# Kernel tuning notes

Hardware: AMD Instinct MI355X
Metric: run time of the kernel (lower is better)

## Reference

```python
import jax, jax.numpy as jnp
import numpy as np

N_NODES = 50000
N_EDGES = 800000
EMB = 100
LAYERS = 3
EPS = 1e-12  # torch F.normalize default eps


def setup_inputs() -> dict:
    key = jax.random.key(0)
    k1, k2, k3, k4 = jax.random.split(key, 4)
    adj_row = jax.random.randint(k1, (N_EDGES,), 0, N_NODES, dtype=jnp.int32)
    adj_col = jax.random.randint(k2, (N_EDGES,), 0, N_NODES, dtype=jnp.int32)
    adj_val = jax.random.uniform(k3, (N_EDGES,), dtype=jnp.float32)
    embedding = jax.random.normal(k4, (N_NODES, EMB), dtype=jnp.float32)
    a = jnp.ones((LAYERS + 1, 1, 1), dtype=jnp.float32)  # init.ones_
    return {"adj_row": adj_row, "adj_col": adj_col, "adj_val": adj_val,
            "embedding": embedding, "a": a}


def reference(adj_row, adj_col, adj_val, embedding, a):
    def spmm(x):
        # sparse.mm(A, x): gather source rows, scale by edge value, scatter-add to dest rows
        return jax.ops.segment_sum(adj_val[:, None] * x[adj_col], adj_row,
                                   num_segments=N_NODES)

    outs = [embedding]
    x = embedding
    for _ in range(LAYERS):
        x = spmm(x)
        outs.append(x)
    final = jnp.stack(outs, axis=0)  # [L+1, N, d]
    # F.normalize(..., dim=-1, p=2): x / max(||x||_2, eps)
    norm = jnp.sqrt(jnp.sum(final * final, axis=-1, keepdims=True))
    final = final / jnp.maximum(norm, EPS)
    return jnp.sum(a * final, axis=0)  # [N, d]
```

## Files before the change

kernel.cpp:

```cpp
#include <hip/hip_runtime.h>
#include <hip/hip_bf16.h>

#define N_NODES 50000
#define N_EDGES 800000
#define EMB 100
#define HALF_EMB 50
#define QEMB 25
#define NORM_EPS 1e-12f
#define BROWS 128
#define NB ((N_NODES + BROWS - 1) / BROWS)
#define CAP 4096
#define EPB 4096
#define SCAT_BLOCKS ((N_EDGES + EPB - 1) / EPB)
#define CONV_BLOCKS 3125

__global__ __launch_bounds__(1024) void scatter_conv(
        const int* __restrict__ adj_row, const int* __restrict__ adj_col,
        const float* __restrict__ adj_val, int* __restrict__ bucket_cnt,
        int2* __restrict__ slab,
        const float* __restrict__ emb, float* __restrict__ norm0,
        __hip_bfloat162* __restrict__ xb) {
    const int t = threadIdx.x;
    if (blockIdx.x >= SCAT_BLOCKS) {
        int wave = (blockIdx.x - SCAT_BLOCKS) * 16 + (t >> 6);
        int lane = t & 63;
        if (wave >= N_NODES) return;
        float2 v = make_float2(0.0f, 0.0f);
        size_t idx = (size_t)wave * HALF_EMB + lane;
        if (lane < HALF_EMB) v = ((const float2*)emb)[idx];
        float s = v.x * v.x + v.y * v.y;
        #pragma unroll
        for (int off = 32; off > 0; off >>= 1) s += __shfl_xor(s, off);
        if (lane == 0) norm0[wave] = sqrtf(s);
        if (lane < HALF_EMB) {
            __hip_bfloat162 b;
            b.x = __float2bfloat16(v.x);
            b.y = __float2bfloat16(v.y);
            xb[idx] = b;
        }
        return;
    }
    __shared__ int hist[NB];
    __shared__ int cur[NB];
    const int base_e = blockIdx.x * EPB;
    for (int i = t; i < NB; i += 1024) hist[i] = 0;
    __syncthreads();
    int rows[EPB / 1024];
    #pragma unroll
    for (int j = 0; j < EPB / 1024; ++j) {
        int e = base_e + j * 1024 + t;
        int r = (e < N_EDGES) ? adj_row[e] : -1;
        rows[j] = r;
        if (r >= 0) atomicAdd(&hist[r >> 7], 1);
    }
    __syncthreads();
    for (int i = t; i < NB; i += 1024) {
        int c = hist[i];
        cur[i] = (c > 0) ? atomicAdd(&bucket_cnt[i], c) : 0;
    }
    __syncthreads();
    #pragma unroll
    for (int j = 0; j < EPB / 1024; ++j) {
        int e = base_e + j * 1024 + t;
        int r = rows[j];
        if (r >= 0) {
            int b = r >> 7;
            int p = atomicAdd(&cur[b], 1);
            unsigned rc = ((unsigned)r << 16) | (unsigned)adj_col[e];
            slab[(size_t)b * CAP + p] = make_int2((int)rc, __float_as_int(adj_val[e]));
        }
    }
}

__global__ __launch_bounds__(1024) void csr_build(
        const int* __restrict__ bucket_cnt, const int2* __restrict__ slab,
        unsigned* __restrict__ csr4, int* __restrict__ row_ptr) {
    __shared__ int2 eds[CAP];
    __shared__ int hist[BROWS];
    __shared__ int incl[BROWS];
    __shared__ int red[1024];
    const int b = blockIdx.x, t = threadIdx.x;
    red[t] = (t < b) ? bucket_cnt[t] : 0;
    __syncthreads();
    #pragma unroll
    for (int off = 512; off > 0; off >>= 1) {
        if (t < off) red[t] += red[t + off];
        __syncthreads();
    }
    const int base = red[0];
    const int cnt = bucket_cnt[b];
    for (int i = t; i < cnt; i += 1024) eds[i] = slab[(size_t)b * CAP + i];
    if (t < BROWS) hist[t] = 0;
    __syncthreads();
    for (int i = t; i < cnt; i += 1024)
        atomicAdd(&hist[(int)(((unsigned)eds[i].x) >> 16) & (BROWS - 1)], 1);
    __syncthreads();
    int v = (t < BROWS) ? hist[t] : 0;
    if (t < BROWS) incl[t] = v;
    __syncthreads();
    #pragma unroll
    for (int off = 1; off < BROWS; off <<= 1) {
        int n = (t >= off && t < BROWS) ? incl[t - off] : 0;
        __syncthreads();
        if (t < BROWS) incl[t] += n;
        __syncthreads();
    }
    int ex = (t < BROWS) ? (incl[t] - v) : 0;
    __syncthreads();
    if (t < BROWS) hist[t] = ex;
    int gr = b * BROWS + t;
    if (t < BROWS && gr < N_NODES) row_ptr[gr] = base + ex;
    if (b == 0 && t == 0) row_ptr[N_NODES] = N_EDGES;
    __syncthreads();
    for (int i = t; i < cnt; i += 1024) {
        int2 e = eds[i];
        int l = (int)(((unsigned)e.x) >> 16) & (BROWS - 1);
        int p = atomicAdd(&hist[l], 1);
        unsigned col = (unsigned)e.x & 0xFFFFu;
        __hip_bfloat16 hv = __float2bfloat16(__int_as_float(e.y));
        unsigned vb = (unsigned)*reinterpret_cast<unsigned short*>(&hv);
        csr4[base + p] = (col << 16) | vb;
    }
}

__device__ inline float4 up4(uint2 u) {
    float4 f;
    f.x = __uint_as_float(u.x << 16);
    f.y = __uint_as_float(u.x & 0xFFFF0000u);
    f.z = __uint_as_float(u.y << 16);
    f.w = __uint_as_float(u.y & 0xFFFF0000u);
    return f;
}

__global__ void spmm_fused(const int* __restrict__ row_ptr,
                           const unsigned* __restrict__ csr4,
                           const uint2* __restrict__ xb,
                           uint2* __restrict__ yb,
                           float* __restrict__ norm_out,
                           const float* __restrict__ a,
                           const uint2* __restrict__ ep0,
                           const uint2* __restrict__ ep1,
                           const float* __restrict__ norms,
                           float* __restrict__ out,
                           int final_layer) {
    int wave = blockIdx.x * (blockDim.x >> 6) + (threadIdx.x >> 6);
    int lane = threadIdx.x & 63;
    if (wave >= N_NODES) return;
    int start = row_ptr[wave];
    int end   = row_ptr[wave + 1];
    int deg   = end - start;
    unsigned myrec = (lane < deg) ? csr4[start + lane] : 0u;
    int h = lane >> 5, c = lane & 31;
    bool act = (c < QEMB);
    float4 acc = make_float4(0.0f, 0.0f, 0.0f, 0.0f);
    int dn  = (deg < 64) ? deg : 64;
    int dn2 = (dn + 1) & ~1;
    int d = 0;
    for (; d + 8 <= dn2; d += 8) {
        unsigned ra = __shfl(myrec, d + h);
        unsigned rb = __shfl(myrec, d + 2 + h);
        unsigned rc = __shfl(myrec, d + 4 + h);
        unsigned rd = __shfl(myrec, d + 6 + h);
        if (act) {
            uint2 ua = xb[(size_t)(ra >> 16) * QEMB + c];
            uint2 ub = xb[(size_t)(rb >> 16) * QEMB + c];
            uint2 uc = xb[(size_t)(rc >> 16) * QEMB + c];
            uint2 ud = xb[(size_t)(rd >> 16) * QEMB + c];
            float va = __uint_as_float(ra << 16);
            float vb = __uint_as_float(rb << 16);
            float vc = __uint_as_float(rc << 16);
            float vd = __uint_as_float(rd << 16);
            float4 fa = up4(ua), fb = up4(ub), fc = up4(uc), fd = up4(ud);
            acc.x += va * fa.x; acc.y += va * fa.y; acc.z += va * fa.z; acc.w += va * fa.w;
            acc.x += vb * fb.x; acc.y += vb * fb.y; acc.z += vb * fb.z; acc.w += vb * fb.w;
            acc.x += vc * fc.x; acc.y += vc * fc.y; acc.z += vc * fc.z; acc.w += vc * fc.w;
            acc.x += vd * fd.x; acc.y += vd * fd.y; acc.z += vd * fd.z; acc.w += vd * fd.w;
        }
    }
    for (; d < dn2; d += 2) {
        unsigned r = __shfl(myrec, d + h);
        if (act) {
            uint2 u = xb[(size_t)(r >> 16) * QEMB + c];
            float v = __uint_as_float(r << 16);
            float4 f = up4(u);
            acc.x += v * f.x; acc.y += v * f.y; acc.z += v * f.z; acc.w += v * f.w;
        }
    }
    for (int e = start + 64; e < end; e += 2) {
        unsigned r = (e + h < end) ? csr4[e + h] : 0u;
        if (act) {
            uint2 u = xb[(size_t)(r >> 16) * QEMB + c];
            float v = __uint_as_float(r << 16);
            float4 f = up4(u);
            acc.x += v * f.x; acc.y += v * f.y; acc.z += v * f.z; acc.w += v * f.w;
        }
    }
    acc.x += __shfl_xor(acc.x, 32);
    acc.y += __shfl_xor(acc.y, 32);
    acc.z += __shfl_xor(acc.z, 32);
    acc.w += __shfl_xor(acc.w, 32);
    float s = 0.0f;
    if (h == 0 && act)
        s = acc.x * acc.x + acc.y * acc.y + acc.z * acc.z + acc.w * acc.w;
    #pragma unroll
    for (int off = 32; off > 0; off >>= 1) s += __shfl_xor(s, off);
    if (!final_layer) {
        if (h == 0 && act) {
            __hip_bfloat16 b0 = __float2bfloat16(acc.x);
            __hip_bfloat16 b1 = __float2bfloat16(acc.y);
            __hip_bfloat16 b2 = __float2bfloat16(acc.z);
            __hip_bfloat16 b3 = __float2bfloat16(acc.w);
            uint2 o;
            o.x = (unsigned)*(unsigned short*)&b0 | ((unsigned)*(unsigned short*)&b1 << 16);
            o.y = (unsigned)*(unsigned short*)&b2 | ((unsigned)*(unsigned short*)&b3 << 16);
            yb[(size_t)wave * QEMB + c] = o;
        }
        if (lane == 0) norm_out[wave] = sqrtf(s);
    } else {
        float s0 = a[0] / fmaxf(norms[wave], NORM_EPS);
        float s1 = a[1] / fmaxf(norms[N_NODES + wave], NORM_EPS);
        float s2 = a[2] / fmaxf(norms[2 * N_NODES + wave], NORM_EPS);
        float s3 = a[3] / fmaxf(sqrtf(s), NORM_EPS);
        if (h == 0 && act) {
            size_t idx = (size_t)wave * QEMB + c;
            float4 f0 = up4(ep0[idx]);
            float4 f1 = up4(ep1[idx]);
            float4 f2 = up4(xb[idx]);
            float4 o;
            o.x = s0 * f0.x + s1 * f1.x + s2 * f2.x + s3 * acc.x;
            o.y = s0 * f0.y + s1 * f1.y + s2 * f2.y + s3 * acc.y;
            o.z = s0 * f0.z + s1 * f1.z + s2 * f2.z + s3 * acc.z;
            o.w = s0 * f0.w + s1 * f1.w + s2 * f2.w + s3 * acc.w;
            ((float4*)out)[idx] = o;
        }
    }
}

extern "C" void kernel_launch(void* const* d_in, const int* in_sizes, int n_in,
                              void* d_out, int out_size, void* d_ws, size_t ws_size,
                              hipStream_t stream) {
    const int*   adj_row   = (const int*)d_in[0];
    const int*   adj_col   = (const int*)d_in[1];
    const float* adj_val   = (const float*)d_in[2];
    const float* embedding = (const float*)d_in[3];
    const float* a         = (const float*)d_in[4];
    float* out = (float*)d_out;

    int2* slab     = (int2*)d_ws;
    unsigned* csr4 = (unsigned*)(slab + (size_t)NB * CAP);
    uint2* xbE = (uint2*)(csr4 + N_EDGES);
    uint2* xb1 = xbE + (size_t)N_NODES * QEMB;
    float* norms = (float*)(xb1 + (size_t)N_NODES * QEMB);
    int* row_ptr    = (int*)(norms + 3 * N_NODES);
    int* bucket_cnt = row_ptr + (N_NODES + 1);
    uint2* xb2 = (uint2*)slab;

    const int node_blocks = (N_NODES + 3) / 4;

    hipMemsetAsync(bucket_cnt, 0, sizeof(int) * NB, stream);
    scatter_conv<<<SCAT_BLOCKS + CONV_BLOCKS, 1024, 0, stream>>>(
        adj_row, adj_col, adj_val, bucket_cnt, slab,
        embedding, norms, (__hip_bfloat162*)xbE);
    csr_build<<<NB, 1024, 0, stream>>>(bucket_cnt, slab, csr4, row_ptr);

    spmm_fused<<<node_blocks, 256, 0, stream>>>(row_ptr, csr4, xbE,
                                                xb1, norms + N_NODES, a,
                                                nullptr, nullptr, nullptr,
                                                nullptr, 0);
    spmm_fused<<<node_blocks, 256, 0, stream>>>(row_ptr, csr4, xb1,
                                                xb2, norms + 2 * N_NODES, a,
                                                nullptr, nullptr, nullptr,
                                                nullptr, 0);
    spmm_fused<<<node_blocks, 256, 0, stream>>>(row_ptr, csr4, xb2,
                                                nullptr, nullptr, a,
                                                xbE, xb1, norms,
                                                out, 1);
}
```

Before: 203.4 us.

## Pad bf16 rows to 128 bytes and accumulate with v_dot2_f32_bf16 over 16-byte loads

The bf16 embedding rows are padded from 100 to 128 elements so each of 16 lanes loads a uint4 (8 values), and a wave now processes four edges at a time instead of two with idle lanes. The inner product pairs two edges per v_dot2_f32_bf16 using byte permutes, which replaces the unpack-and-FMA sequence. csr_build drops its LDS staging and tree reductions in favour of wave shuffles and scans, and scatter uses larger edge chunks per block. The padding adds memory traffic for the zero columns, and reading the slab directly from global memory twice in csr_build may cost some bandwidth.

```diff
diff --git a/kernel.cpp b/kernel.cpp
--- a/kernel.cpp
+++ b/kernel.cpp
@@ -5,14 +5,18 @@
 #define N_EDGES 800000
 #define EMB 100
 #define HALF_EMB 50
-#define QEMB 25
+#define ROW_U4 16
+#define ROW_B2 64
 #define NORM_EPS 1e-12f
 #define BROWS 128
 #define NB ((N_NODES + BROWS - 1) / BROWS)
 #define CAP 4096
-#define EPB 4096
+#define EPB 16384
 #define SCAT_BLOCKS ((N_EDGES + EPB - 1) / EPB)
 #define CONV_BLOCKS 3125
+
+#define SEL_LO 0x01000504u
+#define SEL_HI 0x03020706u
 
 __global__ __launch_bounds__(1024) void scatter_conv(
         const int* __restrict__ adj_row, const int* __restrict__ adj_col,
@@ -26,18 +30,15 @@
         int lane = t & 63;
         if (wave >= N_NODES) return;
         float2 v = make_float2(0.0f, 0.0f);
-        size_t idx = (size_t)wave * HALF_EMB + lane;
-        if (lane < HALF_EMB) v = ((const float2*)emb)[idx];
+        if (lane < HALF_EMB) v = ((const float2*)emb)[(size_t)wave * HALF_EMB + lane];
         float s = v.x * v.x + v.y * v.y;
         #pragma unroll
         for (int off = 32; off > 0; off >>= 1) s += __shfl_xor(s, off);
         if (lane == 0) norm0[wave] = sqrtf(s);
-        if (lane < HALF_EMB) {
-            __hip_bfloat162 b;
-            b.x = __float2bfloat16(v.x);
-            b.y = __float2bfloat16(v.y);
-            xb[idx] = b;
-        }
+        __hip_bfloat162 b;
+        b.x = __float2bfloat16(v.x);
+        b.y = __float2bfloat16(v.y);
+        xb[(size_t)wave * ROW_B2 + lane] = b;
         return;
     }
     __shared__ int hist[NB];
@@ -75,45 +76,49 @@
 __global__ __launch_bounds__(1024) void csr_build(
         const int* __restrict__ bucket_cnt, const int2* __restrict__ slab,
         unsigned* __restrict__ csr4, int* __restrict__ row_ptr) {
-    __shared__ int2 eds[CAP];
     __shared__ int hist[BROWS];
-    __shared__ int incl[BROWS];
-    __shared__ int red[1024];
+    __shared__ int wsum[16];
+    __shared__ int wtot[2];
+    __shared__ int base_sh;
     const int b = blockIdx.x, t = threadIdx.x;
-    red[t] = (t < b) ? bucket_cnt[t] : 0;
-    __syncthreads();
+    const int lane = t & 63, wid = t >> 6;
+    int pv = (t < b) ? bucket_cnt[t] : 0;
     #pragma unroll
-    for (int off = 512; off > 0; off >>= 1) {
-        if (t < off) red[t] += red[t + off];
-        __syncthreads();
-    }
-    const int base = red[0];
+    for (int off = 32; off > 0; off >>= 1) pv += __shfl_xor(pv, off);
+    if (lane == 0) wsum[wid] = pv;
+    if (t < BROWS) hist[t] = 0;
     const int cnt = bucket_cnt[b];
-    for (int i = t; i < cnt; i += 1024) eds[i] = slab[(size_t)b * CAP + i];
-    if (t < BROWS) hist[t] = 0;
-    __syncthreads();
+    __syncthreads();
+    if (t == 0) {
+        int s_ = 0;
+        #pragma unroll
+        for (int i = 0; i < 16; ++i) s_ += wsum[i];
+        base_sh = s_;
+    }
     for (int i = t; i < cnt; i += 1024)
-        atomicAdd(&hist[(int)(((unsigned)eds[i].x) >> 16) & (BROWS - 1)], 1);
-    __syncthreads();
+        atomicAdd(&hist[(int)(((unsigned)slab[(size_t)b * CAP + i].x) >> 16) & (BROWS - 1)], 1);
+    __syncthreads();
+    const int base = base_sh;
     int v = (t < BROWS) ? hist[t] : 0;
-    if (t < BROWS) incl[t] = v;
-    __syncthreads();
+    int sc = v;
     #pragma unroll
-    for (int off = 1; off < BROWS; off <<= 1) {
-        int n = (t >= off && t < BROWS) ? incl[t - off] : 0;
-        __syncthreads();
-        if (t < BROWS) incl[t] += n;
-        __syncthreads();
-    }
-    int ex = (t < BROWS) ? (incl[t] - v) : 0;
-    __syncthreads();
-    if (t < BROWS) hist[t] = ex;
-    int gr = b * BROWS + t;
-    if (t < BROWS && gr < N_NODES) row_ptr[gr] = base + ex;
+    for (int off = 1; off < 64; off <<= 1) {
+        int n = __shfl_up(sc, off);
+        if (lane >= off) sc += n;
+    }
+    if (t < BROWS && lane == 63) wtot[wid] = sc;
+    __syncthreads();
+    if (wid == 1 && t < BROWS) sc += wtot[0];
+    int ex = sc - v;
+    if (t < BROWS) {
+        hist[t] = ex;
+        int gr = b * BROWS + t;
+        if (gr < N_NODES) row_ptr[gr] = base + ex;
+    }
     if (b == 0 && t == 0) row_ptr[N_NODES] = N_EDGES;
     __syncthreads();
     for (int i = t; i < cnt; i += 1024) {
-        int2 e = eds[i];
+        int2 e = slab[(size_t)b * CAP + i];
         int l = (int)(((unsigned)e.x) >> 16) & (BROWS - 1);
         int p = atomicAdd(&hist[l], 1);
         unsigned col = (unsigned)e.x & 0xFFFFu;
@@ -123,23 +128,49 @@
     }
 }
 
-__device__ inline float4 up4(uint2 u) {
-    float4 f;
-    f.x = __uint_as_float(u.x << 16);
-    f.y = __uint_as_float(u.x & 0xFFFF0000u);
-    f.z = __uint_as_float(u.y << 16);
-    f.w = __uint_as_float(u.y & 0xFFFF0000u);
-    return f;
+__device__ inline float dot2b(unsigned a, unsigned b, float c) {
+    float d;
+    asm("v_dot2_f32_bf16 %0, %1, %2, %3" : "=v"(d) : "v"(a), "v"(b), "v"(c));
+    return d;
+}
+
+__device__ inline void dot8pair(unsigned ra, unsigned rb, uint4 ua, uint4 ub,
+                                float4& accL, float4& accH) {
+    unsigned vp = __builtin_amdgcn_perm(ra, rb, SEL_LO);
+    accL.x = dot2b(vp, __builtin_amdgcn_perm(ua.x, ub.x, SEL_LO), accL.x);
+    accL.y = dot2b(vp, __builtin_amdgcn_perm(ua.x, ub.x, SEL_HI), accL.y);
+    accL.z = dot2b(vp, __builtin_amdgcn_perm(ua.y, ub.y, SEL_LO), accL.z);
+    accL.w = dot2b(vp, __builtin_amdgcn_perm(ua.y, ub.y, SEL_HI), accL.w);
+    accH.x = dot2b(vp, __builtin_amdgcn_perm(ua.z, ub.z, SEL_LO), accH.x);
+    accH.y = dot2b(vp, __builtin_amdgcn_perm(ua.z, ub.z, SEL_HI), accH.y);
+    accH.z = dot2b(vp, __builtin_amdgcn_perm(ua.w, ub.w, SEL_LO), accH.z);
+    accH.w = dot2b(vp, __builtin_amdgcn_perm(ua.w, ub.w, SEL_HI), accH.w);
+}
+
+__device__ inline void up8(uint4 u, float4& lo, float4& hi) {
+    lo.x = __uint_as_float(u.x << 16);
+    lo.y = __uint_as_float(u.x & 0xFFFF0000u);
+    lo.z = __uint_as_float(u.y << 16);
+    lo.w = __uint_as_float(u.y & 0xFFFF0000u);
+    hi.x = __uint_as_float(u.z << 16);
+    hi.y = __uint_as_float(u.z & 0xFFFF0000u);
+    hi.z = __uint_as_float(u.w << 16);
+    hi.w = __uint_as_float(u.w & 0xFFFF0000u);
+}
+
+__device__ inline unsigned pack2(float a, float b) {
+    __hip_bfloat16 x = __float2bfloat16(a), y = __float2bfloat16(b);
+    return (unsigned)*(unsigned short*)&x | ((unsigned)*(unsigned short*)&y << 16);
 }
 
 __global__ void spmm_fused(const int* __restrict__ row_ptr,
                            const unsigned* __restrict__ csr4,
-                           const uint2* __restrict__ xb,
-                           uint2* __restrict__ yb,
+                           const uint4* __restrict__ xb,
+                           uint4* __restrict__ yb,
                            float* __restrict__ norm_out,
                            const float* __restrict__ a,
-                           const uint2* __restrict__ ep0,
-                           const uint2* __restrict__ ep1,
+                           const uint4* __restrict__ ep0,
+                           const uint4* __restrict__ ep1,
                            const float* __restrict__ norms,
                            float* __restrict__ out,
                            int final_layer) {
@@ -150,70 +181,69 @@
     int end   = row_ptr[wave + 1];
     int deg   = end - start;
     unsigned myrec = (lane < deg) ? csr4[start + lane] : 0u;
-    int h = lane >> 5, c = lane & 31;
-    bool act = (c < QEMB);
-    float4 acc = make_float4(0.0f, 0.0f, 0.0f, 0.0f);
+    int g = lane >> 4, c = lane & 15;
+    float4 accL = make_float4(0.0f, 0.0f, 0.0f, 0.0f);
+    float4 accH = make_float4(0.0f, 0.0f, 0.0f, 0.0f);
     int dn  = (deg < 64) ? deg : 64;
-    int dn2 = (dn + 1) & ~1;
+    int dn4 = (dn + 3) & ~3;
     int d = 0;
-    for (; d + 8 <= dn2; d += 8) {
-        unsigned ra = __shfl(myrec, d + h);
-        unsigned rb = __shfl(myrec, d + 2 + h);
-        unsigned rc = __shfl(myrec, d + 4 + h);
-        unsigned rd = __shfl(myrec, d + 6 + h);
-        if (act) {
-            uint2 ua = xb[(size_t)(ra >> 16) * QEMB + c];
-            uint2 ub = xb[(size_t)(rb >> 16) * QEMB + c];
-            uint2 uc = xb[(size_t)(rc >> 16) * QEMB + c];
-            uint2 ud = xb[(size_t)(rd >> 16) * QEMB + c];
-            float va = __uint_as_float(ra << 16);
-            float vb = __uint_as_float(rb << 16);
-            float vc = __uint_as_float(rc << 16);
-            float vd = __uint_as_float(rd << 16);
-            float4 fa = up4(ua), fb = up4(ub), fc = up4(uc), fd = up4(ud);
-            acc.x += va * fa.x; acc.y += va * fa.y; acc.z += va * fa.z; acc.w += va * fa.w;
-            acc.x += vb * fb.x; acc.y += vb * fb.y; acc.z += vb * fb.z; acc.w += vb * fb.w;
-            acc.x += vc * fc.x; acc.y += vc * fc.y; acc.z += vc * fc.z; acc.w += vc * fc.w;
-            acc.x += vd * fd.x; acc.y += vd * fd.y; acc.z += vd * fd.z; acc.w += vd * fd.w;
-        }
-    }
-    for (; d < dn2; d += 2) {
-        unsigned r = __shfl(myrec, d + h);
-        if (act) {
-            uint2 u = xb[(size_t)(r >> 16) * QEMB + c];
-            float v = __uint_as_float(r << 16);
-            float4 f = up4(u);
-            acc.x += v * f.x; acc.y += v * f.y; acc.z += v * f.z; acc.w += v * f.w;
-        }
-    }
-    for (int e = start + 64; e < end; e += 2) {
-        unsigned r = (e + h < end) ? csr4[e + h] : 0u;
-        if (act) {
-            uint2 u = xb[(size_t)(r >> 16) * QEMB + c];
-            float v = __uint_as_float(r << 16);
-            float4 f = up4(u);
-            acc.x += v * f.x; acc.y += v * f.y; acc.z += v * f.z; acc.w += v * f.w;
-        }
-    }
-    acc.x += __shfl_xor(acc.x, 32);
-    acc.y += __shfl_xor(acc.y, 32);
-    acc.z += __shfl_xor(acc.z, 32);
-    acc.w += __shfl_xor(acc.w, 32);
-    float s = 0.0f;
-    if (h == 0 && act)
-        s = acc.x * acc.x + acc.y * acc.y + acc.z * acc.z + acc.w * acc.w;
-    #pragma unroll
-    for (int off = 32; off > 0; off >>= 1) s += __shfl_xor(s, off);
+    for (; d + 16 <= dn4; d += 16) {
+        unsigned ra = __shfl(myrec, d + g);
+        unsigned rb = __shfl(myrec, d + 4 + g);
+        unsigned rc = __shfl(myrec, d + 8 + g);
+        unsigned rd = __shfl(myrec, d + 12 + g);
+        uint4 ua = xb[(size_t)(ra >> 16) * ROW_U4 + c];
+        uint4 ub = xb[(size_t)(rb >> 16) * ROW_U4 + c];
+        uint4 uc = xb[(size_t)(rc >> 16) * ROW_U4 + c];
+        uint4 ud = xb[(size_t)(rd >> 16) * ROW_U4 + c];
+        dot8pair(ra, rb, ua, ub, accL, accH);
+        dot8pair(rc, rd, uc, ud, accL, accH);
+    }
+    for (; d + 8 <= dn4; d += 8) {
+        unsigned ra = __shfl(myrec, d + g);
+        unsigned rb = __shfl(myrec, d + 4 + g);
+        uint4 ua = xb[(size_t)(ra >> 16) * ROW_U4 + c];
+        uint4 ub = xb[(size_t)(rb >> 16) * ROW_U4 + c];
+        dot8pair(ra, rb, ua, ub, accL, accH);
+    }
+    for (; d < dn4; d += 4) {
+        unsigned r = __shfl(myrec, d + g);
+        uint4 u = xb[(size_t)(r >> 16) * ROW_U4 + c];
+        float v = __uint_as_float(r << 16);
+        float4 l, h;
+        up8(u, l, h);
+        accL.x += v * l.x; accL.y += v * l.y; accL.z += v * l.z; accL.w += v * l.w;
+        accH.x += v * h.x; accH.y += v * h.y; accH.z += v * h.z; accH.w += v * h.w;
+    }
+    for (int e = start + 64; e < end; e += 4) {
+        unsigned r = (e + g < end) ? csr4[e + g] : 0u;
+        uint4 u = xb[(size_t)(r >> 16) * ROW_U4 + c];
+        float v = __uint_as_float(r << 16);
+        float4 l, h;
+        up8(u, l, h);
+        accL.x += v * l.x; accL.y += v * l.y; accL.z += v * l.z; accL.w += v * l.w;
+        accH.x += v * h.x; accH.y += v * h.y; accH.z += v * h.z; accH.w += v * h.w;
+    }
+    accL.x += __shfl_xor(accL.x, 16); accL.x += __shfl_xor(accL.x, 32);
+    accL.y += __shfl_xor(accL.y, 16); accL.y += __shfl_xor(accL.y, 32);
+    accL.z += __shfl_xor(accL.z, 16); accL.z += __shfl_xor(accL.z, 32);
+    accL.w += __shfl_xor(accL.w, 16); accL.w += __shfl_xor(accL.w, 32);
+    accH.x += __shfl_xor(accH.x, 16); accH.x += __shfl_xor(accH.x, 32);
+    accH.y += __shfl_xor(accH.y, 16); accH.y += __shfl_xor(accH.y, 32);
+    accH.z += __shfl_xor(accH.z, 16); accH.z += __shfl_xor(accH.z, 32);
+    accH.w += __shfl_xor(accH.w, 16); accH.w += __shfl_xor(accH.w, 32);
+    float s = accL.x * accL.x + accL.y * accL.y + accL.z * accL.z + accL.w * accL.w
+            + accH.x * accH.x + accH.y * accH.y + accH.z * accH.z + accH.w * accH.w;
+    s += __shfl_xor(s, 1); s += __shfl_xor(s, 2);
+    s += __shfl_xor(s, 4); s += __shfl_xor(s, 8);
     if (!final_layer) {
-        if (h == 0 && act) {
-            __hip_bfloat16 b0 = __float2bfloat16(acc.x);
-            __hip_bfloat16 b1 = __float2bfloat16(acc.y);
-            __hip_bfloat16 b2 = __float2bfloat16(acc.z);
-            __hip_bfloat16 b3 = __float2bfloat16(acc.w);
-            uint2 o;
-            o.x = (unsigned)*(unsigned short*)&b0 | ((unsigned)*(unsigned short*)&b1 << 16);
-            o.y = (unsigned)*(unsigned short*)&b2 | ((unsigned)*(unsigned short*)&b3 << 16);
-            yb[(size_t)wave * QEMB + c] = o;
+        if (g == 0) {
+            uint4 o;
+            o.x = pack2(accL.x, accL.y);
+            o.y = pack2(accL.z, accL.w);
+            o.z = pack2(accH.x, accH.y);
+            o.w = pack2(accH.z, accH.w);
+            yb[(size_t)wave * ROW_U4 + c] = o;
         }
         if (lane == 0) norm_out[wave] = sqrtf(s);
     } else {
@@ -221,17 +251,29 @@
         float s1 = a[1] / fmaxf(norms[N_NODES + wave], NORM_EPS);
         float s2 = a[2] / fmaxf(norms[2 * N_NODES + wave], NORM_EPS);
         float s3 = a[3] / fmaxf(sqrtf(s), NORM_EPS);
-        if (h == 0 && act) {
-            size_t idx = (size_t)wave * QEMB + c;
-            float4 f0 = up4(ep0[idx]);
-            float4 f1 = up4(ep1[idx]);
-            float4 f2 = up4(xb[idx]);
-            float4 o;
-            o.x = s0 * f0.x + s1 * f1.x + s2 * f2.x + s3 * acc.x;
-            o.y = s0 * f0.y + s1 * f1.y + s2 * f2.y + s3 * acc.y;
-            o.z = s0 * f0.z + s1 * f1.z + s2 * f2.z + s3 * acc.z;
-            o.w = s0 * f0.w + s1 * f1.w + s2 * f2.w + s3 * acc.w;
-            ((float4*)out)[idx] = o;
+        if (g == 0 && c < 13) {
+            size_t idx = (size_t)wave * ROW_U4 + c;
+            float4 f0l, f0h, f1l, f1h, f2l, f2h;
+            up8(ep0[idx], f0l, f0h);
+            up8(ep1[idx], f1l, f1h);
+            up8(xb[idx],  f2l, f2h);
+            float4 o0, o1;
+            o0.x = s0 * f0l.x + s1 * f1l.x + s2 * f2l.x + s3 * accL.x;
+            o0.y = s0 * f0l.y + s1 * f1l.y + s2 * f2l.y + s3 * accL.y;
+            o0.z = s0 * f0l.z + s1 * f1l.z + s2 * f2l.z + s3 * accL.z;
+            o0.w = s0 * f0l.w + s1 * f1l.w + s2 * f2l.w + s3 * accL.w;
+            o1.x = s0 * f0h.x + s1 * f1h.x + s2 * f2h.x + s3 * accH.x;
+            o1.y = s0 * f0h.y + s1 * f1h.y + s2 * f2h.y + s3 * accH.y;
+            o1.z = s0 * f0h.z + s1 * f1h.z + s2 * f2h.z + s3 * accH.z;
+            o1.w = s0 * f0h.w + s1 * f1h.w + s2 * f2h.w + s3 * accH.w;
+            float4* out4 = (float4*)out;
+            size_t fb = (size_t)wave * 25;
+            if (c < 12) {
+                out4[fb + 2 * c]     = o0;
+                out4[fb + 2 * c + 1] = o1;
+            } else {
+                out4[fb + 24] = o0;
+            }
         }
     }
 }
@@ -248,12 +290,12 @@
 
     int2* slab     = (int2*)d_ws;
     unsigned* csr4 = (unsigned*)(slab + (size_t)NB * CAP);
-    uint2* xbE = (uint2*)(csr4 + N_EDGES);
-    uint2* xb1 = xbE + (size_t)N_NODES * QEMB;
-    float* norms = (float*)(xb1 + (size_t)N_NODES * QEMB);
+    uint4* xbE = (uint4*)(csr4 + N_EDGES);
+    uint4* xb1 = xbE + (size_t)N_NODES * ROW_U4;
+    float* norms = (float*)(xb1 + (size_t)N_NODES * ROW_U4);
     int* row_ptr    = (int*)(norms + 3 * N_NODES);
     int* bucket_cnt = row_ptr + (N_NODES + 1);
-    uint2* xb2 = (uint2*)slab;
+    uint4* xb2 = (uint4*)slab;
 
     const int node_blocks = (N_NODES + 3) / 4;
 
```

Result: slower. 216.4 us (+6.4%).
